# Optimization experiments

Hardware: AMD Instinct MI355X
Metric: run time of the kernel (lower is better)

The kernel has to match this reference:

```python
import math
import jax, jax.numpy as jnp
import numpy as np

C = 8.0  # decay constant from __init__
_MIN_RAD, _MAX_RAD = 0.9, 0.999


def block_diag_linear(x, w):
    # x: (B,T,D), w: (H, bs, bs) with D = H*bs
    B, T, D = x.shape
    H, bs, _ = w.shape
    xh = x.reshape(B, T, H, bs)
    return jnp.einsum('bthd,hde->bthe', xh, w).reshape(B, T, D)


def linear_scan(a, b):
    # h_t = a_t * h_{t-1} + b_t, h_{-1}=0, via associative scan:
    # (a1,b1) o (a2,b2) = (a1*a2, a2*b1 + b2)
    def op(l, r):
        a1, b1 = l
        a2, b2 = r
        return (a1 * a2, a2 * b1 + b2)
    return jax.lax.associative_scan(op, (a, b), axis=1)[1]


def setup_inputs() -> dict:
    key = jax.random.key(0)
    k1, k2, k3, k4 = jax.random.split(key, 4)
    B, T, D, H = 4, 4096, 1024, 8
    bs = D // H
    x = jax.random.normal(k1, (B, T, D), dtype=jnp.float32)
    std = 1.0 / math.sqrt(bs)
    w_in = jax.random.normal(k2, (H, bs, bs), dtype=jnp.float32) * std
    w_a = jax.random.normal(k3, (H, bs, bs), dtype=jnp.float32) * std
    # a_param init: softplus^{-1} of uniform in [-log(max_rad)/c, -log(min_rad)/c]
    sp = jax.random.uniform(k4, (D,), dtype=jnp.float32,
                            minval=-math.log(_MAX_RAD) / C,
                            maxval=-math.log(_MIN_RAD) / C)
    a_param = jnp.log(jnp.exp(sp) - 1.0 + 1e-8)
    return {"x": x, "a_param": a_param, "w_in": w_in, "w_a": w_a}


def reference(x, a_param, w_in, w_a):
    # RG-LRU forward with h_prev = None
    gate_x = jax.nn.sigmoid(block_diag_linear(x, w_in))  # input gate i_t
    gate_a = jax.nn.sigmoid(block_diag_linear(x, w_a))   # recurrence gate r_t
    log_a = -C * jax.nn.softplus(a_param) * gate_a       # (B,T,D)
    a = jnp.exp(log_a)
    multiplier = jnp.sqrt(1.0 - jnp.exp(2.0 * log_a))    # sqrt(1 - a^2)
    b = multiplier * (gate_x * x)
    y = linear_scan(a, b)                                 # (B,T,D)
    h_last = y[:, -1, :]
    return y, h_last
```

## Files before the change

kernel.cpp:

```cpp
#include <hip/hip_runtime.h>

#define B_ 4
#define T_ 4096
#define D_ 1024
#define H_ 8
#define M_ (B_*T_)

typedef unsigned short u16;
typedef unsigned int u32;
typedef __attribute__((ext_vector_type(8))) short s16x8;
typedef __attribute__((ext_vector_type(4))) float f32x4;

#define LOG2E 1.4426950408889634f

__device__ __forceinline__ float ex2(float x){
#if __has_builtin(__builtin_amdgcn_exp2f)
  return __builtin_amdgcn_exp2f(x);
#else
  return exp2f(x);
#endif
}
__device__ __forceinline__ float rcpf(float x){
#if __has_builtin(__builtin_amdgcn_rcpf)
  return __builtin_amdgcn_rcpf(x);
#else
  return __fdividef(1.0f, x);
#endif
}
__device__ __forceinline__ float bf2f(u16 u){
  union { u32 i; float f; } v; v.i = ((u32)u) << 16; return v.f;
}
__device__ __forceinline__ u16 f2bf(float f){
  union { float f; u32 i; } v; v.f = f;
  u32 i = v.i;
  return (u16)((i + 0x7FFFu + ((i >> 16) & 1u)) >> 16);
}
__device__ __forceinline__ float sigf(float z){
  return rcpf(1.0f + ex2(-LOG2E * z));
}
__device__ __forceinline__ s16x8 cvt8(float4 a, float4 b){
  s16x8 r;
  r[0] = (short)(__float_as_uint(a.x) >> 16);
  r[1] = (short)(__float_as_uint(a.y) >> 16);
  r[2] = (short)(__float_as_uint(a.z) >> 16);
  r[3] = (short)(__float_as_uint(a.w) >> 16);
  r[4] = (short)(__float_as_uint(b.x) >> 16);
  r[5] = (short)(__float_as_uint(b.y) >> 16);
  r[6] = (short)(__float_as_uint(b.z) >> 16);
  r[7] = (short)(__float_as_uint(b.w) >> 16);
  return r;
}

__global__ __launch_bounds__(256) void k0_transpose(const float* __restrict__ w_in,
                                                    const float* __restrict__ w_a,
                                                    u16* __restrict__ wt){
  __shared__ float ls[128][132];
  const int blk = blockIdx.x;
  const float* src = (blk < 8 ? w_in : w_a) + (size_t)(blk & 7) * 128 * 128;
  u16* dst = wt + (size_t)blk * 128 * 128;
  const int tid = threadIdx.x;
  const int r0 = tid >> 5;
  const int c0 = (tid & 31) * 4;
  #pragma unroll
  for (int it = 0; it < 16; ++it){
    int r = r0 + it * 8;
    *(float4*)(&ls[r][c0]) = *(const float4*)(src + r * 128 + c0);
  }
  __syncthreads();
  #pragma unroll
  for (int it = 0; it < 16; ++it){
    int e = r0 + it * 8;
    ushort4 u;
    u.x = f2bf(ls[c0 + 0][e]);
    u.y = f2bf(ls[c0 + 1][e]);
    u.z = f2bf(ls[c0 + 2][e]);
    u.w = f2bf(ls[c0 + 3][e]);
    *(ushort4*)(dst + e * 128 + c0) = u;
  }
}

__global__ __launch_bounds__(256, 2) void k1_gemm_scan(
    const float* __restrict__ x, const float* __restrict__ a_param,
    const u16* __restrict__ wt, u32* __restrict__ pack,
    float* __restrict__ Ablk, float* __restrict__ Yblk)
{
  __shared__ __align__(16) union SMem {
    u16 w[2][64][136];
    u32 p[128 * 68];
  } SU;
  __shared__ float waveC[4][64][2];
  __shared__ float aspS[64];

  const int blk = blockIdx.x;
  const int hh  = blk & 15;
  const int h = hh >> 1, eh = hh & 1;
  const int mbg = blk >> 4;
  const int batch = mbg >> 5;
  const int tb    = mbg & 31;
  const int mbase = mbg * 128;
  const int tid = threadIdx.x;
  const int wv = tid >> 6, lane = tid & 63;
  const int q = lane >> 4, l = lane & 15;

  {
    uint4 wbuf[8];
    #pragma unroll
    for (int it = 0; it < 8; ++it){
      int idx = tid + it * 256;
      int row = idx >> 4;
      int mat = row >> 6, e = row & 63;
      int c8 = (idx & 15) * 8;
      wbuf[it] = *(const uint4*)(wt + (size_t)mat * (8 * 128 * 128)
                                  + (h * 128 + eh * 64 + e) * 128 + c8);
    }
    #pragma unroll
    for (int it = 0; it < 8; ++it){
      int idx = tid + it * 256;
      int row = idx >> 4;
      int c8 = (idx & 15) * 8;
      *(uint4*)(&SU.w[0][0][0] + row * 136 + c8) = wbuf[it];
    }
  }

  const float* xr0 = x + (size_t)(mbase + wv * 32 + l) * D_ + h * 128;
  const float* xr1 = xr0 + 16 * D_;
  float4 A0[4][2], A1[4][2];
  #pragma unroll
  for (int kb = 0; kb < 4; ++kb){
    int ko = kb * 32 + q * 8;
    A0[kb][0] = *(const float4*)(xr0 + ko);
    A0[kb][1] = *(const float4*)(xr0 + ko + 4);
    A1[kb][0] = *(const float4*)(xr1 + ko);
    A1[kb][1] = *(const float4*)(xr1 + ko + 4);
  }
  if (tid < 64)
    aspS[tid] = 8.0f * log1pf(__expf(a_param[h * 128 + eh * 64 + tid]));
  __syncthreads();

  f32x4 accX[2][4], accG[2][4];
  #pragma unroll
  for (int mt = 0; mt < 2; ++mt)
    #pragma unroll
    for (int nt = 0; nt < 4; ++nt){ accX[mt][nt] = (f32x4)0.0f; accG[mt][nt] = (f32x4)0.0f; }

  #pragma unroll
  for (int kb = 0; kb < 4; ++kb){
    const int ko = kb * 32 + q * 8;
    s16x8 a0 = cvt8(A0[kb][0], A0[kb][1]);
    s16x8 a1 = cvt8(A1[kb][0], A1[kb][1]);
    #pragma unroll
    for (int nt = 0; nt < 4; ++nt){
      s16x8 bi = *(const s16x8*)(&SU.w[0][nt * 16 + l][ko]);
      s16x8 ba = *(const s16x8*)(&SU.w[1][nt * 16 + l][ko]);
      accX[0][nt] = __builtin_amdgcn_mfma_f32_16x16x32_bf16(a0, bi, accX[0][nt], 0, 0, 0);
      accX[1][nt] = __builtin_amdgcn_mfma_f32_16x16x32_bf16(a1, bi, accX[1][nt], 0, 0, 0);
      accG[0][nt] = __builtin_amdgcn_mfma_f32_16x16x32_bf16(a0, ba, accG[0][nt], 0, 0, 0);
      accG[1][nt] = __builtin_amdgcn_mfma_f32_16x16x32_bf16(a1, ba, accG[1][nt], 0, 0, 0);
    }
  }

  float av[2][4][4], bv[2][4][4];
  #pragma unroll
  for (int mt = 0; mt < 2; ++mt){
    #pragma unroll
    for (int nt = 0; nt < 4; ++nt){
      const int el = nt * 16 + l;
      const int col = eh * 64 + el;
      const float asp = aspS[el];
      #pragma unroll
      for (int r = 0; r < 4; ++r){
        const int row = wv * 32 + mt * 16 + q * 4 + r;
        float gx = sigf(accX[mt][nt][r]);
        float ga = sigf(accG[mt][nt][r]);
        float la = -asp * ga;
        float a  = ex2(LOG2E * la);
        float mult = sqrtf(fmaxf(1.0f - a * a, 0.0f));
        float xv = x[(size_t)(mbase + row) * D_ + h * 128 + col];
        av[mt][nt][r] = a;
        bv[mt][nt][r] = mult * gx * xv;
      }
    }
  }

  float preA[2][4], preY[2][4];
  #pragma unroll
  for (int nt = 0; nt < 4; ++nt){
    const int col = nt * 16 + l;
    float S0A = 1.0f, S0Y = 0.0f;
    #pragma unroll
    for (int mt = 0; mt < 2; ++mt){
      float a0 = av[mt][nt][0], a1 = av[mt][nt][1], a2 = av[mt][nt][2], a3 = av[mt][nt][3];
      float b0 = bv[mt][nt][0], b1 = bv[mt][nt][1], b2 = bv[mt][nt][2], b3 = bv[mt][nt][3];
      float TA = (a0 * a1) * (a2 * a3);
      float TY = fmaf(a3, fmaf(a2, fmaf(a1, b0, b1), b2), b3);
      float QA0 = __shfl(TA, l,      64), QY0 = __shfl(TY, l,      64);
      float QA1 = __shfl(TA, l + 16, 64), QY1 = __shfl(TY, l + 16, 64);
      float QA2 = __shfl(TA, l + 32, 64), QY2 = __shfl(TY, l + 32, 64);
      float QA3 = __shfl(TA, l + 48, 64), QY3 = __shfl(TY, l + 48, 64);
      float P1A = QA0,       P1Y = QY0;
      float P2A = P1A * QA1, P2Y = fmaf(QA1, P1Y, QY1);
      float P3A = P2A * QA2, P3Y = fmaf(QA2, P2Y, QY2);
      float QpA = (q == 0) ? 1.0f : ((q == 1) ? P1A : ((q == 2) ? P2A : P3A));
      float QpY = (q == 0) ? 0.0f : ((q == 1) ? P1Y : ((q == 2) ? P2Y : P3Y));
      float S16A = P3A * QA3, S16Y = fmaf(QA3, P3Y, QY3);
      float MA = (mt == 0) ? 1.0f : S0A;
      float MY = (mt == 0) ? 0.0f : S0Y;
      preA[mt][nt] = MA * QpA;
      preY[mt][nt] = fmaf(QpA, MY, QpY);
      if (mt == 0){ S0A = S16A; S0Y = S16Y; }
      else {
        float WA = S0A * S16A, WY = fmaf(S16A, S0Y, S16Y);
        if (lane < 16){ waveC[wv][col][0] = WA; waveC[wv][col][1] = WY; }
      }
    }
  }
  __syncthreads();

  float wpA[4], wpY[4];
  #pragma unroll
  for (int nt = 0; nt < 4; ++nt){
    int col = nt * 16 + l;
    float A = 1.0f, Y = 0.0f;
    #pragma unroll
    for (int w2 = 0; w2 < 3; ++w2){
      if (w2 < wv){
        float cA = waveC[w2][col][0], cY = waveC[w2][col][1];
        Y = fmaf(cA, Y, cY);
        A = A * cA;
      }
    }
    wpA[nt] = A; wpY[nt] = Y;
  }

  if (wv == 0){
    const int col = lane;
    float bA = waveC[0][col][0], bY = waveC[0][col][1];
    float cA1 = waveC[1][col][0], cY1 = waveC[1][col][1];
    float cA2 = waveC[2][col][0], cY2 = waveC[2][col][1];
    float cA3 = waveC[3][col][0], cY3 = waveC[3][col][1];
    bY = fmaf(cA1, bY, cY1); bA *= cA1;
    bY = fmaf(cA2, bY, cY2); bA *= cA2;
    bY = fmaf(cA3, bY, cY3); bA *= cA3;
    int gi = (batch * 32 + tb) * D_ + h * 128 + eh * 64 + col;
    Ablk[gi] = bA;
    Yblk[gi] = bY;
  }

  #pragma unroll
  for (int nt = 0; nt < 4; ++nt){
    const int col = nt * 16 + l;
    float basev = wpY[nt];
    #pragma unroll
    for (int mt = 0; mt < 2; ++mt){
      float v  = fmaf(preA[mt][nt], basev, preY[mt][nt]);
      float cA = wpA[nt] * preA[mt][nt];
      const int R0 = wv * 32 + mt * 16 + q * 4;
      #pragma unroll
      for (int r = 0; r < 4; ++r){
        v  = fmaf(av[mt][nt][r], v, bv[mt][nt][r]);
        cA = cA * av[mt][nt][r];
        SU.p[(R0 + r) * 68 + col] = (u32)f2bf(v) | ((u32)f2bf(cA) << 16);
      }
    }
  }
  __syncthreads();

  {
    u32* pg = pack + (size_t)mbase * D_ + h * 128 + eh * 64;
    #pragma unroll
    for (int it = 0; it < 8; ++it){
      int idx = tid + it * 256;
      int row = idx >> 4;
      int c4 = (idx & 15) * 4;
      uint4 v = *(uint4*)(&SU.p[row * 68 + c4]);
      *(uint4*)(pg + (size_t)row * D_ + c4) = v;
    }
  }
}

__global__ __launch_bounds__(256) void k2_scan_agg(const float* __restrict__ Ablk,
                                                   const float* __restrict__ Yblk,
                                                   float* __restrict__ hin,
                                                   float* __restrict__ hlast){
  const int g = blockIdx.x * 256 + threadIdx.x;
  const int batch = g >> 10, d = g & 1023;
  float hcur = 0.0f;
  #pragma unroll
  for (int t = 0; t < 32; ++t){
    int gi = (batch * 32 + t) * D_ + d;
    float A = Ablk[gi], Y = Yblk[gi];
    hin[gi] = hcur;
    hcur = fmaf(A, hcur, Y);
  }
  hlast[batch * D_ + d] = hcur;
}

__global__ __launch_bounds__(256) void k3_fixup(const u32* pack,
                                               const float* __restrict__ hin,
                                               float* y_out){
  const int cg = blockIdx.x;
  const int r0 = cg * 16;
  const int batch = r0 >> 12;
  const int tb = (r0 & (T_ - 1)) >> 7;
  const int d0 = threadIdx.x * 4;
  float4 hv = *(const float4*)(&hin[(batch * 32 + tb) * D_ + d0]);
  #pragma unroll
  for (int t = 0; t < 16; ++t){
    int idx = (r0 + t) * D_ + d0;
    uint4 w = *(const uint4*)(&pack[idx]);
    float4 yv;
    yv.x = fmaf(bf2f((u16)(w.x >> 16)), hv.x, bf2f((u16)(w.x & 0xFFFFu)));
    yv.y = fmaf(bf2f((u16)(w.y >> 16)), hv.y, bf2f((u16)(w.y & 0xFFFFu)));
    yv.z = fmaf(bf2f((u16)(w.z >> 16)), hv.z, bf2f((u16)(w.z & 0xFFFFu)));
    yv.w = fmaf(bf2f((u16)(w.w >> 16)), hv.w, bf2f((u16)(w.w & 0xFFFFu)));
    *(float4*)(&y_out[idx]) = yv;
  }
}

extern "C" void kernel_launch(void* const* d_in, const int* in_sizes, int n_in,
                              void* d_out, int out_size, void* d_ws, size_t ws_size,
                              hipStream_t stream) {
  const float* x    = (const float*)d_in[0];
  const float* ap   = (const float*)d_in[1];
  const float* w_in = (const float*)d_in[2];
  const float* w_a  = (const float*)d_in[3];
  float* y = (float*)d_out;
  float* hlast = y + (size_t)B_ * T_ * D_;
  u32* pack = (u32*)d_out;

  char* ws = (char*)d_ws;
  u16*   wt   = (u16*)(ws);
  float* Ablk = (float*)(ws + 524288);
  float* Yblk = (float*)(ws + 1048576);
  float* hin  = (float*)(ws + 1572864);

  k0_transpose<<<16, 256, 0, stream>>>(w_in, w_a, wt);
  k1_gemm_scan<<<128 * 16, 256, 0, stream>>>(x, ap, wt, pack, Ablk, Yblk);
  k2_scan_agg<<<16, 256, 0, stream>>>(Ablk, Yblk, hin, hlast);
  k3_fixup<<<1024, 256, 0, stream>>>(pack, hin, y);
}
```

Before: 177.7 us.

## Fold block-carry aggregation into fixup kernel and raise k1 occupancy hint

Removes the separate serial carry-aggregation kernel. Each fixup block now recomputes its incoming state by scanning the per-block A/Y summaries of all earlier time blocks, and the last block of each batch writes h_last. This drops one launch and the serial low-parallelism k2, at the cost of redundant summary loads, up to 31 per block. It also raises k1's launch_bounds min-blocks from 2 to 4, which may force register spilling.

```diff
diff --git a/kernel.cpp b/kernel.cpp
--- a/kernel.cpp
+++ b/kernel.cpp
@@ -79,7 +79,7 @@
   }
 }
 
-__global__ __launch_bounds__(256, 2) void k1_gemm_scan(
+__global__ __launch_bounds__(256, 4) void k1_gemm_scan(
     const float* __restrict__ x, const float* __restrict__ a_param,
     const u16* __restrict__ wt, u32* __restrict__ pack,
     float* __restrict__ Ablk, float* __restrict__ Yblk)
@@ -278,42 +278,41 @@
   }
 }
 
-__global__ __launch_bounds__(256) void k2_scan_agg(const float* __restrict__ Ablk,
-                                                   const float* __restrict__ Yblk,
-                                                   float* __restrict__ hin,
-                                                   float* __restrict__ hlast){
-  const int g = blockIdx.x * 256 + threadIdx.x;
-  const int batch = g >> 10, d = g & 1023;
-  float hcur = 0.0f;
-  #pragma unroll
-  for (int t = 0; t < 32; ++t){
-    int gi = (batch * 32 + t) * D_ + d;
-    float A = Ablk[gi], Y = Yblk[gi];
-    hin[gi] = hcur;
-    hcur = fmaf(A, hcur, Y);
-  }
-  hlast[batch * D_ + d] = hcur;
-}
-
 __global__ __launch_bounds__(256) void k3_fixup(const u32* pack,
-                                               const float* __restrict__ hin,
-                                               float* y_out){
+                                               const float* __restrict__ Ablk,
+                                               const float* __restrict__ Yblk,
+                                               float* y_out, float* hlast){
   const int cg = blockIdx.x;
   const int r0 = cg * 16;
   const int batch = r0 >> 12;
   const int tb = (r0 & (T_ - 1)) >> 7;
   const int d0 = threadIdx.x * 4;
-  float4 hv = *(const float4*)(&hin[(batch * 32 + tb) * D_ + d0]);
+
+  float4 hv; hv.x = 0.0f; hv.y = 0.0f; hv.z = 0.0f; hv.w = 0.0f;
+  for (int t = 0; t < tb; ++t){
+    int gi = (batch * 32 + t) * D_ + d0;
+    float4 A = *(const float4*)(&Ablk[gi]);
+    float4 Y = *(const float4*)(&Yblk[gi]);
+    hv.x = fmaf(A.x, hv.x, Y.x);
+    hv.y = fmaf(A.y, hv.y, Y.y);
+    hv.z = fmaf(A.z, hv.z, Y.z);
+    hv.w = fmaf(A.w, hv.w, Y.w);
+  }
+
+  float4 yv;
   #pragma unroll
   for (int t = 0; t < 16; ++t){
     int idx = (r0 + t) * D_ + d0;
     uint4 w = *(const uint4*)(&pack[idx]);
-    float4 yv;
     yv.x = fmaf(bf2f((u16)(w.x >> 16)), hv.x, bf2f((u16)(w.x & 0xFFFFu)));
     yv.y = fmaf(bf2f((u16)(w.y >> 16)), hv.y, bf2f((u16)(w.y & 0xFFFFu)));
     yv.z = fmaf(bf2f((u16)(w.z >> 16)), hv.z, bf2f((u16)(w.z & 0xFFFFu)));
     yv.w = fmaf(bf2f((u16)(w.w >> 16)), hv.w, bf2f((u16)(w.w & 0xFFFFu)));
     *(float4*)(&y_out[idx]) = yv;
+  }
+
+  if (((r0 + 16) & (T_ - 1)) == 0){
+    *(float4*)(&hlast[batch * D_ + d0]) = yv;
   }
 }
 
@@ -332,10 +331,8 @@
   u16*   wt   = (u16*)(ws);
   float* Ablk = (float*)(ws + 524288);
   float* Yblk = (float*)(ws + 1048576);
-  float* hin  = (float*)(ws + 1572864);
 
   k0_transpose<<<16, 256, 0, stream>>>(w_in, w_a, wt);
   k1_gemm_scan<<<128 * 16, 256, 0, stream>>>(x, ap, wt, pack, Ablk, Yblk);
-  k2_scan_agg<<<16, 256, 0, stream>>>(Ablk, Yblk, hin, hlast);
-  k3_fixup<<<1024, 256, 0, stream>>>(pack, hin, y);
-}
+  k3_fixup<<<1024, 256, 0, stream>>>(pack, Ablk, Yblk, y, hlast);
+}
```

New measurement: 198.7 us. +11.8%, slower.
